# Kernel tuning notes

Measured on AMD Instinct MI355X. Metric: run time of the kernel, lower is better.

The kernel has to match this reference:

```python
import jax, jax.numpy as jnp
import numpy as np

B, S, D = 32, 512, 512
H, DK, DV, DFF = 8, 64, 64, 2048
TEMP = float(np.sqrt(DK))  # d_k ** 0.5
COS_EPS = 1e-8             # torch.cosine_similarity eps
LN_EPS = 1e-5


def _layernorm(x, g, b):
    mu = jnp.mean(x, axis=-1, keepdims=True)
    var = jnp.var(x, axis=-1, keepdims=True)
    return (x - mu) * jax.lax.rsqrt(var + LN_EPS) * g + b


def setup_inputs() -> dict:
    key = jax.random.key(0)
    ks = jax.random.split(key, 12)
    s = 0.02
    return {
        "x": jax.random.normal(ks[0], (B, S, D), dtype=jnp.float32),
        "w_q": jax.random.normal(ks[1], (D, H * DK), dtype=jnp.float32) * s,
        "w_k": jax.random.normal(ks[2], (D, H * DK), dtype=jnp.float32) * s,
        "w_v": jax.random.normal(ks[3], (D, H * DV), dtype=jnp.float32) * s,
        "w_o": jax.random.normal(ks[4], (H * DV, D), dtype=jnp.float32) * s,
        "w_ff1": jax.random.normal(ks[5], (D, DFF), dtype=jnp.float32) * s,
        "b_ff1": jnp.zeros((DFF,), dtype=jnp.float32),
        "w_ff2": jax.random.normal(ks[6], (DFF, D), dtype=jnp.float32) * s,
        "b_ff2": jnp.zeros((D,), dtype=jnp.float32),
        "g1": jnp.ones((D,), dtype=jnp.float32),
        "b1": jnp.zeros((D,), dtype=jnp.float32),
        "g2": jnp.ones((D,), dtype=jnp.float32),
        "b2": jnp.zeros((D,), dtype=jnp.float32),
    }


def reference(x, w_q, w_k, w_v, w_o, w_ff1, b_ff1, w_ff2, b_ff2, g1, b1, g2, b2):
    b, s, _ = x.shape
    # projections -> [b, h, s, d]
    q = (x @ w_q).reshape(b, s, H, DK).transpose(0, 2, 1, 3)
    k = (x @ w_k).reshape(b, s, H, DK).transpose(0, 2, 1, 3)
    v = (x @ w_v).reshape(b, s, H, DV).transpose(0, 2, 1, 3)
    # cosine-similarity attention: dot(q,k) / max(||q||*||k||, eps) / temperature
    scores = jnp.einsum("bhqd,bhkd->bhqk", q, k)
    nq = jnp.linalg.norm(q, axis=-1)  # [b,h,s]
    nk = jnp.linalg.norm(k, axis=-1)
    denom = jnp.maximum(nq[:, :, :, None] * nk[:, :, None, :], COS_EPS)
    attn = jax.nn.softmax(scores / denom / TEMP, axis=-1)
    out = jnp.einsum("bhqk,bhkd->bhqd", attn, v)  # [b,h,s,dv]
    out = out.transpose(0, 2, 1, 3).reshape(b, s, H * DV) @ w_o
    # residual + LN1
    h1 = _layernorm(x + out, g1, b1)
    # FFN
    ffn = jax.nn.relu(h1 @ w_ff1 + b_ff1) @ w_ff2 + b_ff2
    # residual + LN2
    return _layernorm(h1 + ffn, g2, b2)
```

## Files before the change

kernel.cpp:

```cpp
#include <hip/hip_runtime.h>
#include <cmath>

typedef __bf16 bf16x8 __attribute__((ext_vector_type(8)));
typedef __bf16 bf16x4 __attribute__((ext_vector_type(4)));
typedef float  floatx4 __attribute__((ext_vector_type(4)));

#define LN_EPS 1e-5f
#define INV_TEMP 0.125f

static const int Mrows = 16384;

__device__ __forceinline__ void gload_lds16(const void* g, void* l) {
  __builtin_amdgcn_global_load_lds(
      (const __attribute__((address_space(1))) void*)g,
      (__attribute__((address_space(3))) void*)l, 16, 0, 0);
}

__global__ __launch_bounds__(256) void prep_kernel(const float* __restrict__ x, __bf16* __restrict__ xb,
                                                   const float* __restrict__ wq, const float* __restrict__ wk,
                                                   const float* __restrict__ wv, const float* __restrict__ wo,
                                                   const float* __restrict__ wff1, const float* __restrict__ wff2,
                                                   __bf16* __restrict__ tq, __bf16* __restrict__ tk,
                                                   __bf16* __restrict__ tv, __bf16* __restrict__ to_,
                                                   __bf16* __restrict__ tff1, __bf16* __restrict__ tff2) {
  const int bid = blockIdx.x, tid = threadIdx.x;
  if (bid < 8192) {
    int i = bid * 256 + tid;
    float4 v = ((const float4*)x)[i];
    __bf16* d = xb + i * 4;
    d[0] = (__bf16)v.x; d[1] = (__bf16)v.y; d[2] = (__bf16)v.z; d[3] = (__bf16)v.w;
    return;
  }
  __shared__ __bf16 til[64][72];
  int t = bid - 8192;
  const float* src; __bf16* dst; int R, C, bx, by;
  if (t < 256) {
    int w = t >> 6, tt = t & 63;
    const float* srcs[4] = {wq, wk, wv, wo};
    __bf16* dsts[4] = {tq, tk, tv, to_};
    src = srcs[w]; dst = dsts[w]; R = 512; C = 512; bx = tt & 7; by = tt >> 3;
  } else if (t < 512) {
    int tt = t - 256;
    src = wff1; dst = tff1; R = 512; C = 2048; bx = tt & 31; by = tt >> 5;
  } else {
    int tt = t - 512;
    src = wff2; dst = tff2; R = 2048; C = 512; bx = tt & 7; by = tt >> 3;
  }
  const float* s = src + (size_t)(by * 64) * C + bx * 64;
  int r = tid >> 4, c4 = (tid & 15) * 4;
  for (int p = 0; p < 4; ++p) {
    int rr = r + p * 16;
    float4 v = *(const float4*)(s + (size_t)rr * C + c4);
    til[c4 + 0][rr] = (__bf16)v.x;
    til[c4 + 1][rr] = (__bf16)v.y;
    til[c4 + 2][rr] = (__bf16)v.z;
    til[c4 + 3][rr] = (__bf16)v.w;
  }
  __syncthreads();
  __bf16* d = dst + (size_t)(bx * 64) * R + by * 64;
  int orow = tid >> 3, oc8 = (tid & 7) * 8;
  for (int p = 0; p < 2; ++p) {
    int rr = orow + p * 32;
    *(bf16x8*)(d + (size_t)rr * R + oc8) = *(const bf16x8*)(&til[rr][oc8]);
  }
}

template <int EPI, int NBN, int NDIM, int KDIM, int NKS>
__global__ __launch_bounds__(512, 2) void gemm256(const __bf16* __restrict__ A,
                                                  const __bf16* __restrict__ Bt,
                                                  __bf16* __restrict__ Cv,
                                                  const float* __restrict__ bias,
                                                  float* __restrict__ norms,
                                                  __bf16* __restrict__ vtg) {
  __shared__ __align__(16) char smem[131072];
  const int tid = threadIdx.x;
  const int wave = tid >> 6, lane = tid & 63;
  const int l15 = lane & 15, quad = lane >> 4;
  const int wm = wave >> 2, wn = wave & 3;

  constexpr int NBM = Mrows / 256;
  constexpr int NBLK = NBM * NBN * NKS;
  constexpr int KS = KDIM / NKS;
  constexpr int NTH = KS / 32;

  int id = blockIdx.x;
  int t = (id & 7) * (NBLK >> 3) + (id >> 3);
  const int ks = t / (NBM * NBN);
  t -= ks * (NBM * NBN);
  const int nblk = t % NBN, mblk = t / NBN;
  const int m0 = mblk * 256, n0 = nblk * 256;
  const __bf16* Ab = A + (size_t)ks * KS;
  const __bf16* Bb = Bt + (size_t)ks * KS;
  __bf16* Cw = Cv + (size_t)ks * Mrows * NDIM;
  (void)bias;

  const int wq = wave & 3, isB = wave >> 2;
  const int l3 = lane >> 3, sl7 = lane & 7;
  const int slog = sl7 ^ l3;
  const int wbit = slog & 1, kseg = slog >> 1;
  const int rl = l3 * 2 + wbit;
  const __bf16* sbase = (isB ? Bb + (size_t)(n0 + wq * 64 + rl) * KDIM
                             : Ab + (size_t)(m0 + wq * 64 + rl) * KDIM) + kseg * 8;
  const int ldob = isB * 16384 + wq * 4096 + lane * 16;

  const int rsw = (l15 >> 1) * 128 + ((((quad << 1) | (l15 & 1)) ^ (l15 >> 1)) * 16);
  const int wmBase = wm * 8192;
  const int wnBase = wn * 4096;

  floatx4 zero = {0.f, 0.f, 0.f, 0.f};
  floatx4 acc[8][4];
#pragma unroll
  for (int i = 0; i < 8; ++i)
#pragma unroll
    for (int j = 0; j < 4; ++j) acc[i][j] = zero;

#define STAGEH(h)                                                            \
  {                                                                          \
    _Pragma("unroll") for (int j = 0; j < 4; ++j)                            \
        gload_lds16(sbase + (size_t)j * (16 * KDIM) + (h) * 32,              \
                    smem + ((h) & 3) * 32768 + ldob + j * 1024);             \
  }

#define PHASE(h, DOSTAGE, VM)                                                \
  {                                                                          \
    asm volatile("s_waitcnt vmcnt(" #VM ")" ::: "memory");                   \
    __builtin_amdgcn_s_barrier();                                            \
    const char* slotp = smem + ((h) & 3) * 32768;                            \
    bf16x8 aF[8], bF[4];                                                     \
    _Pragma("unroll") for (int i = 0; i < 8; ++i)                            \
      aF[i] = *(const bf16x8*)(slotp + wmBase + i * 1024 + rsw);             \
    _Pragma("unroll") for (int j = 0; j < 4; ++j)                            \
      bF[j] = *(const bf16x8*)(slotp + 16384 + wnBase + j * 1024 + rsw);     \
    if (DOSTAGE) STAGEH((h) + 3);                                            \
    __builtin_amdgcn_s_setprio(1);                                           \
    _Pragma("unroll") for (int i = 0; i < 8; ++i)                            \
      _Pragma("unroll") for (int j = 0; j < 4; ++j)                          \
        acc[i][j] = __builtin_amdgcn_mfma_f32_16x16x32_bf16(aF[i], bF[j],    \
                                                            acc[i][j], 0, 0, 0); \
    __builtin_amdgcn_s_setprio(0);                                           \
  }

  STAGEH(0); STAGEH(1); STAGEH(2);

  for (int h = 0; h <= NTH - 4; ++h) PHASE(h, 1, 8);
  PHASE(NTH - 3, 0, 8);
  PHASE(NTH - 2, 0, 4);
  PHASE(NTH - 1, 0, 0);

#undef STAGEH
#undef PHASE

  if (EPI == 4) {
    int head_global = (n0 + wn * 64) >> 6;
    int kind = head_global >> 3;
    if (kind < 2) {
      int h = head_global & 7;
#pragma unroll
      for (int ii = 0; ii < 8; ++ii)
#pragma unroll
        for (int r = 0; r < 4; ++r) {
          float sq = 0.f;
#pragma unroll
          for (int jj = 0; jj < 4; ++jj) {
            float v = acc[ii][jj][r];
            sq += v * v;
          }
          for (int m = 1; m < 16; m <<= 1) sq += __shfl_xor(sq, m, 64);
          if (l15 == 0) {
            int arow = m0 + wm * 128 + ii * 16 + quad * 4 + r;
            int bb = arow >> 9, ss = arow & 511;
            norms[kind * 131072 + ((bb << 3) + h) * 512 + ss] = rsqrtf(sq);
          }
        }
    } else {
      const int PADT = 136;
      __bf16* Ct = (__bf16*)smem;
      int bb = m0 >> 9, s0r = m0 & 511;
#pragma unroll
      for (int hh = 0; hh < 2; ++hh) {
        __builtin_amdgcn_s_barrier();
        if (wm == hh) {
#pragma unroll
          for (int ii = 0; ii < 8; ++ii)
#pragma unroll
            for (int jj = 0; jj < 4; ++jj) {
              bf16x4 pk;
#pragma unroll
              for (int r = 0; r < 4; ++r) pk[r] = (__bf16)acc[ii][jj][r];
              *(bf16x4*)(Ct + (wn * 64 + jj * 16 + l15) * PADT + ii * 16 + quad * 4) = pk;
            }
        }
        __builtin_amdgcn_s_barrier();
#pragma unroll
        for (int p = 0; p < 8; ++p) {
          int c = p * 32 + (tid >> 4);
          int s8 = (tid & 15) * 8;
          int h = ((n0 + c) >> 6) & 7, d = c & 63;
          *(bf16x8*)(vtg + ((size_t)(((bb << 3) + h) * 64 + d)) * 512 + s0r + hh * 128 + s8) =
              *(const bf16x8*)(Ct + c * PADT + s8);
        }
      }
      return;
    }
  }

  const int PADC = 264;
  __bf16* Cs = (__bf16*)smem;
  float bv[4];
  if (EPI == 2) {
#pragma unroll
    for (int j = 0; j < 4; ++j) bv[j] = bias[n0 + wn * 64 + j * 16 + l15];
  }
#pragma unroll
  for (int hh = 0; hh < 2; ++hh) {
    __builtin_amdgcn_s_barrier();
    if (wm == hh) {
#pragma unroll
      for (int i = 0; i < 8; ++i)
#pragma unroll
        for (int j = 0; j < 4; ++j)
#pragma unroll
          for (int r = 0; r < 4; ++r) {
            float v = acc[i][j][r];
            if (EPI == 2) {
              v += bv[j];
              v = v > 0.f ? v : 0.f;
            }
            Cs[(i * 16 + quad * 4 + r) * PADC + wn * 64 + j * 16 + l15] = (__bf16)v;
          }
    }
    __builtin_amdgcn_s_barrier();
#pragma unroll
    for (int p = 0; p < 8; ++p) {
      int rowl = p * 16 + (tid >> 5);
      int c8 = (tid & 31) * 8;
      *(bf16x8*)(Cw + (size_t)(m0 + hh * 128 + rowl) * NDIM + n0 + c8) =
          *(const bf16x8*)(Cs + rowl * PADC + c8);
    }
  }
}

__global__ __launch_bounds__(256) void attn_kernel(const __bf16* __restrict__ qkv,
                                                   const __bf16* __restrict__ vtg,
                                                   const float* __restrict__ norms,
                                                   __bf16* __restrict__ out) {
  __shared__ __align__(16) __bf16 Ks[64 * 64];
  __shared__ __align__(16) __bf16 Vs[64 * 64];
  __shared__ __align__(16) __bf16 P2[4][16 * 72];
  const int tid = threadIdx.x, wave = tid >> 6, lane = tid & 63;
  const int l15 = lane & 15, quad = lane >> 4;
  const int bh = blockIdx.x & 255;
  const int qq = blockIdx.x >> 8;
  const int b = bh >> 3, h = bh & 7;
  const int qbase = qq * 128 + wave * 32;
  const int rs = lane >> 3;
  const int swz_st = ((lane & 7) ^ rs) * 8;
  const int s7 = l15 & 7;

  const __bf16* Qb = qkv + (size_t)(b * 512) * 1536 + h * 64;
  const __bf16* Kb = Qb + 512;
  const __bf16* Vtb = vtg + (size_t)bh * 32768;
  const float* nkinv = norms + 131072 + bh * 512;
  const float* nqinv = norms + bh * 512;
  __bf16* Pw = P2[wave];

  bf16x8 aq[2][2];
  float cq[2];
  for (int ch = 0; ch < 2; ++ch) {
    int qrow = qbase + ch * 16;
    aq[ch][0] = *(const bf16x8*)(Qb + (size_t)(qrow + l15) * 1536 + quad * 8);
    aq[ch][1] = *(const bf16x8*)(Qb + (size_t)(qrow + l15) * 1536 + 32 + quad * 8);
    cq[ch] = nqinv[qrow + l15] * INV_TEMP;
  }

  floatx4 zero = {0.f, 0.f, 0.f, 0.f};
  floatx4 o[2][4];
  float lsum[2] = {0.f, 0.f};
  for (int ch = 0; ch < 2; ++ch)
    for (int jd = 0; jd < 4; ++jd) o[ch][jd] = zero;

  for (int kt = 0; kt < 8; ++kt) {
    int s0 = kt * 64;
    __syncthreads();
    for (int c = 0; c < 4; ++c) {
      int g = wave * 4 + c;
      const __bf16* src;
      __bf16* dst;
      if (g < 8) {
        int sk = g * 8 + rs;
        src = Kb + (size_t)(s0 + sk) * 1536 + swz_st;
        dst = Ks + g * 512;
      } else {
        int g2 = g - 8;
        int d = g2 * 8 + rs;
        src = Vtb + (size_t)d * 512 + s0 + swz_st;
        dst = Vs + g2 * 512;
      }
      gload_lds16(src, dst + lane * 8);
    }
    __syncthreads();

    for (int ch = 0; ch < 2; ++ch) {
      floatx4 z[4];
      for (int j = 0; j < 4; ++j) {
        int r64 = (j * 16 + l15) * 64;
        bf16x8 k0 = *(const bf16x8*)(Ks + r64 + ((quad ^ s7) * 8));
        bf16x8 k1 = *(const bf16x8*)(Ks + r64 + (((4 + quad) ^ s7) * 8));
        floatx4 zz = zero;
        zz = __builtin_amdgcn_mfma_f32_16x16x32_bf16(k0, aq[ch][0], zz, 0, 0, 0);
        zz = __builtin_amdgcn_mfma_f32_16x16x32_bf16(k1, aq[ch][1], zz, 0, 0, 0);
        z[j] = zz;
      }
      for (int j = 0; j < 4; ++j) {
        floatx4 nk4 = *(const floatx4*)(nkinv + s0 + j * 16 + quad * 4);
        bf16x4 pk;
        for (int r = 0; r < 4; ++r) {
          float p = __expf(z[j][r] * cq[ch] * nk4[r]);
          lsum[ch] += p;
          pk[r] = (__bf16)p;
        }
        *(bf16x4*)(Pw + l15 * 72 + j * 16 + quad * 4) = pk;
      }
      bf16x8 ap0 = *(const bf16x8*)(Pw + l15 * 72 + quad * 8);
      bf16x8 ap1 = *(const bf16x8*)(Pw + l15 * 72 + 32 + quad * 8);
      for (int jd = 0; jd < 4; ++jd) {
        int r64 = (jd * 16 + l15) * 64;
        bf16x8 v0 = *(const bf16x8*)(Vs + r64 + ((quad ^ s7) * 8));
        bf16x8 v1 = *(const bf16x8*)(Vs + r64 + (((4 + quad) ^ s7) * 8));
        o[ch][jd] = __builtin_amdgcn_mfma_f32_16x16x32_bf16(v0, ap0, o[ch][jd], 0, 0, 0);
        o[ch][jd] = __builtin_amdgcn_mfma_f32_16x16x32_bf16(v1, ap1, o[ch][jd], 0, 0, 0);
      }
    }
  }

  for (int ch = 0; ch < 2; ++ch) {
    float s = lsum[ch];
    s += __shfl_xor(s, 16, 64);
    s += __shfl_xor(s, 32, 64);
    float inv = __builtin_amdgcn_rcpf(s);
    int q = qbase + ch * 16 + l15;
    __bf16* op = out + (size_t)(b * 512 + q) * 512 + h * 64;
    for (int jd = 0; jd < 4; ++jd) {
      bf16x4 pk;
      for (int r = 0; r < 4; ++r) pk[r] = (__bf16)(o[ch][jd][r] * inv);
      *(bf16x4*)(op + jd * 16 + quad * 4) = pk;
    }
  }
}

template <bool X1BF, bool WF, bool WB, bool DUAL>
__global__ __launch_bounds__(256) void resid_ln(const float* __restrict__ X1f,
                                                const __bf16* __restrict__ X1b,
                                                const __bf16* __restrict__ X2,
                                                const __bf16* __restrict__ X2b,
                                                const float* __restrict__ bias,
                                                const float* __restrict__ g,
                                                const float* __restrict__ be,
                                                float* __restrict__ outf,
                                                __bf16* __restrict__ outb) {
  int row = blockIdx.x * 4 + (threadIdx.x >> 6);
  int lane = threadIdx.x & 63;
  float v[8];
  bf16x8 b8 = *(const bf16x8*)(X2 + (size_t)row * 512 + lane * 8);
  if (X1BF) {
    bf16x8 a = *(const bf16x8*)(X1b + (size_t)row * 512 + lane * 8);
    for (int i = 0; i < 8; ++i) v[i] = (float)a[i] + (float)b8[i];
  } else {
    const float4* r1 = (const float4*)(X1f + (size_t)row * 512);
    float4 a0 = r1[lane * 2], a1 = r1[lane * 2 + 1];
    v[0] = a0.x; v[1] = a0.y; v[2] = a0.z; v[3] = a0.w;
    v[4] = a1.x; v[5] = a1.y; v[6] = a1.z; v[7] = a1.w;
    for (int i = 0; i < 8; ++i) v[i] += (float)b8[i];
  }
  if (DUAL) {
    bf16x8 c8 = *(const bf16x8*)(X2b + (size_t)row * 512 + lane * 8);
    for (int i = 0; i < 8; ++i) v[i] += (float)c8[i];
  }
  if (bias) {
    const float* bp = bias + lane * 8;
    for (int i = 0; i < 8; ++i) v[i] += bp[i];
  }
  float s = 0.f, sq = 0.f;
  for (int i = 0; i < 8; ++i) {
    s += v[i];
    sq += v[i] * v[i];
  }
  for (int m = 1; m < 64; m <<= 1) {
    s += __shfl_xor(s, m, 64);
    sq += __shfl_xor(sq, m, 64);
  }
  float mean = s * (1.f / 512.f);
  float var = sq * (1.f / 512.f) - mean * mean;
  float rstd = rsqrtf(var + LN_EPS);
  const float* gp = g + lane * 8;
  const float* bp2 = be + lane * 8;
  float o[8];
  for (int i = 0; i < 8; ++i) o[i] = (v[i] - mean) * rstd * gp[i] + bp2[i];
  if (WF) {
    float4 w0 = {o[0], o[1], o[2], o[3]}, w1 = {o[4], o[5], o[6], o[7]};
    ((float4*)(outf + (size_t)row * 512))[lane * 2] = w0;
    ((float4*)(outf + (size_t)row * 512))[lane * 2 + 1] = w1;
  }
  if (WB) {
    __bf16 tmp[8];
    for (int i = 0; i < 8; ++i) tmp[i] = (__bf16)o[i];
    *(bf16x8*)(outb + (size_t)row * 512 + lane * 8) = *(bf16x8*)tmp;
  }
}

extern "C" void kernel_launch(void* const* d_in, const int* in_sizes, int n_in,
                              void* d_out, int out_size, void* d_ws, size_t ws_size,
                              hipStream_t stream) {
  const float* x     = (const float*)d_in[0];
  const float* w_q   = (const float*)d_in[1];
  const float* w_k   = (const float*)d_in[2];
  const float* w_v   = (const float*)d_in[3];
  const float* w_o   = (const float*)d_in[4];
  const float* w_ff1 = (const float*)d_in[5];
  const float* b_ff1 = (const float*)d_in[6];
  const float* w_ff2 = (const float*)d_in[7];
  const float* b_ff2 = (const float*)d_in[8];
  const float* g1    = (const float*)d_in[9];
  const float* b1    = (const float*)d_in[10];
  const float* g2    = (const float*)d_in[11];
  const float* b2    = (const float*)d_in[12];
  float* out = (float*)d_out;

  char* ws = (char*)d_ws;
  size_t off = 0;
  auto alloc = [&](size_t bytes) -> void* {
    void* p = ws + off;
    off += (bytes + 255) & ~(size_t)255;
    return p;
  };
  __bf16* xb     = (__bf16*)alloc((size_t)Mrows * 512 * 2);
  __bf16* wt_qkv = (__bf16*)alloc((size_t)1536 * 512 * 2);
  __bf16* wt_o   = (__bf16*)alloc((size_t)512 * 512 * 2);
  __bf16* wt_ff1 = (__bf16*)alloc((size_t)2048 * 512 * 2);
  __bf16* wt_ff2 = (__bf16*)alloc((size_t)512 * 2048 * 2);
  __bf16* qkv    = (__bf16*)alloc((size_t)Mrows * 1536 * 2);
  float*  norms  = (float*)alloc((size_t)262144 * 4);
  __bf16* attn   = (__bf16*)alloc((size_t)Mrows * 512 * 2);
  __bf16* projb  = (__bf16*)alloc((size_t)Mrows * 512 * 2);
  __bf16* h1b    = (__bf16*)alloc((size_t)Mrows * 512 * 2);
  __bf16* mid    = (__bf16*)alloc((size_t)Mrows * 2048 * 2);
  __bf16* vtg    = mid;
  __bf16* wo_p   = mid;
  __bf16* f2o    = attn;

  prep_kernel<<<8960, 256, 0, stream>>>(x, xb, w_q, w_k, w_v, w_o, w_ff1, w_ff2,
                                        wt_qkv, wt_qkv + 512 * 512, wt_qkv + 2 * 512 * 512,
                                        wt_o, wt_ff1, wt_ff2);

  gemm256<4, 6, 1536, 512, 1><<<dim3(384), 512, 0, stream>>>(xb, wt_qkv, qkv, nullptr,
                                                             norms, vtg);
  attn_kernel<<<dim3(1024), 256, 0, stream>>>(qkv, vtg, norms, attn);
  gemm256<0, 2, 512, 512, 2><<<dim3(256), 512, 0, stream>>>(attn, wt_o, wo_p, nullptr,
                                                            nullptr, nullptr);
  resid_ln<false, false, true, true><<<4096, 256, 0, stream>>>(x, nullptr, wo_p,
                                                               wo_p + (size_t)Mrows * 512,
                                                               nullptr, g1, b1, nullptr, h1b);
  gemm256<2, 8, 2048, 512, 1><<<dim3(512), 512, 0, stream>>>(h1b, wt_ff1, mid, b_ff1,
                                                             nullptr, nullptr);
  gemm256<0, 2, 512, 2048, 2><<<dim3(256), 512, 0, stream>>>(mid, wt_ff2, f2o, nullptr,
                                                             nullptr, nullptr);
  resid_ln<true, true, false, true><<<4096, 256, 0, stream>>>(nullptr, h1b, f2o,
                                                              f2o + (size_t)Mrows * 512,
                                                              b_ff2, g2, b2, out, nullptr);
}
```

Measured before the change: 333.7 us.

## Double-buffer GEMM register fragments and rework LDS swizzle pattern

Restructures the bf16 GEMM main loop so the LDS fragments for the next K-slice are read into a second register set before the MFMAs of the current slice are issued. This is meant to overlap LDS read latency with matrix-core work. The LDS row/k-segment XOR swizzle is also changed on both the staging and read side, aiming to reduce bank conflicts. In exchange the kernel holds twice the fragment registers, which could lower occupancy or cause spills, and the loop now assumes an even number of middle iterations.

```diff
diff --git a/kernel.cpp b/kernel.cpp
--- a/kernel.cpp
+++ b/kernel.cpp
@@ -95,17 +95,16 @@
   (void)bias;
 
   const int wq = wave & 3, isB = wave >> 2;
-  const int l3 = lane >> 3, sl7 = lane & 7;
-  const int slog = sl7 ^ l3;
-  const int wbit = slog & 1, kseg = slog >> 1;
-  const int rl = l3 * 2 + wbit;
-  const __bf16* sbase = (isB ? Bb + (size_t)(n0 + wq * 64 + rl) * KDIM
-                             : Ab + (size_t)(m0 + wq * 64 + rl) * KDIM) + kseg * 8;
+  const int l3 = lane >> 3, s_ = lane & 7;
+  const int rowst = wq * 64 + l3 * 2 + (s_ >> 2);
+  const int ksw = (s_ & 3) ^ (l3 & 3);
+  const __bf16* sbase = (isB ? Bb + (size_t)(n0 + rowst) * KDIM
+                             : Ab + (size_t)(m0 + rowst) * KDIM) + ksw * 8;
   const int ldob = isB * 16384 + wq * 4096 + lane * 16;
 
-  const int rsw = (l15 >> 1) * 128 + ((((quad << 1) | (l15 & 1)) ^ (l15 >> 1)) * 16);
-  const int wmBase = wm * 8192;
-  const int wnBase = wn * 4096;
+  const int rsw = (l15 >> 1) * 128 + (((l15 & 1) * 4 + (quad ^ ((l15 >> 1) & 3))) * 16);
+  const int aoff = wm * 8192;
+  const int boff = 16384 + wn * 4096;
 
   floatx4 zero = {0.f, 0.f, 0.f, 0.f};
   floatx4 acc[8][4];
@@ -113,6 +112,8 @@
   for (int i = 0; i < 8; ++i)
 #pragma unroll
     for (int j = 0; j < 4; ++j) acc[i][j] = zero;
+
+  bf16x8 fA0[8], fB0[4], fA1[8], fB1[4];
 
 #define STAGEH(h)                                                            \
   {                                                                          \
@@ -121,33 +122,54 @@
                     smem + ((h) & 3) * 32768 + ldob + j * 1024);             \
   }
 
-#define PHASE(h, DOSTAGE, VM)                                                \
+#define READF(S, h)                                                          \
   {                                                                          \
-    asm volatile("s_waitcnt vmcnt(" #VM ")" ::: "memory");                   \
-    __builtin_amdgcn_s_barrier();                                            \
-    const char* slotp = smem + ((h) & 3) * 32768;                            \
-    bf16x8 aF[8], bF[4];                                                     \
+    const char* sp = smem + ((h) & 3) * 32768;                               \
     _Pragma("unroll") for (int i = 0; i < 8; ++i)                            \
-      aF[i] = *(const bf16x8*)(slotp + wmBase + i * 1024 + rsw);             \
+      fA##S[i] = *(const bf16x8*)(sp + aoff + i * 1024 + rsw);               \
     _Pragma("unroll") for (int j = 0; j < 4; ++j)                            \
-      bF[j] = *(const bf16x8*)(slotp + 16384 + wnBase + j * 1024 + rsw);     \
-    if (DOSTAGE) STAGEH((h) + 3);                                            \
+      fB##S[j] = *(const bf16x8*)(sp + boff + j * 1024 + rsw);               \
+  }
+
+#define MFMAS(S)                                                             \
+  {                                                                          \
     __builtin_amdgcn_s_setprio(1);                                           \
     _Pragma("unroll") for (int i = 0; i < 8; ++i)                            \
       _Pragma("unroll") for (int j = 0; j < 4; ++j)                          \
-        acc[i][j] = __builtin_amdgcn_mfma_f32_16x16x32_bf16(aF[i], bF[j],    \
+        acc[i][j] = __builtin_amdgcn_mfma_f32_16x16x32_bf16(fA##S[i], fB##S[j], \
                                                             acc[i][j], 0, 0, 0); \
     __builtin_amdgcn_s_setprio(0);                                           \
   }
 
+#define PHASE(h, C, N, VM, DOPF, DOSTAGE)                                    \
+  {                                                                          \
+    if (DOPF) {                                                              \
+      asm volatile("s_waitcnt vmcnt(" #VM ")" ::: "memory");                 \
+      __builtin_amdgcn_s_barrier();                                          \
+      READF(N, (h) + 1);                                                     \
+    }                                                                        \
+    if (DOSTAGE) STAGEH((h) + 3);                                            \
+    MFMAS(C);                                                                \
+  }
+
   STAGEH(0); STAGEH(1); STAGEH(2);
-
-  for (int h = 0; h <= NTH - 4; ++h) PHASE(h, 1, 8);
-  PHASE(NTH - 3, 0, 8);
-  PHASE(NTH - 2, 0, 4);
-  PHASE(NTH - 1, 0, 0);
+  asm volatile("s_waitcnt vmcnt(8)" ::: "memory");
+  __builtin_amdgcn_s_barrier();
+  READF(0, 0);
+
+  for (int h2 = 0; h2 < (NTH - 4) / 2; ++h2) {
+    int h = h2 * 2;
+    PHASE(h,     0, 1, 4, 1, 1);
+    PHASE(h + 1, 1, 0, 4, 1, 1);
+  }
+  PHASE(NTH - 4, 0, 1, 4, 1, 1);
+  PHASE(NTH - 3, 1, 0, 4, 1, 0);
+  PHASE(NTH - 2, 0, 1, 0, 1, 0);
+  MFMAS(1);
 
 #undef STAGEH
+#undef READF
+#undef MFMAS
 #undef PHASE
 
   if (EPI == 4) {
```

Measured after the change: 332.2 us. Within noise of the previous version (-0.4%).
